# Optimization experiments

Measured on AMD Instinct MI355X. Metric: run time of the kernel, lower is better.

The kernel has to match this reference:

```python
import jax, jax.numpy as jnp
import numpy as np

N = 1_000_000
H = 128
G = 4096


def setup_inputs() -> dict:
    key = jax.random.key(0)
    k1, k2, k3, k4 = jax.random.split(key, 4)
    x = jax.random.normal(k1, (N, H), dtype=jnp.float32)
    batch = jnp.sort(jax.random.randint(k2, (N,), 0, G, dtype=jnp.int64))
    w1 = jax.random.normal(k3, (H, H), dtype=jnp.float32) * 0.05
    b1 = jnp.zeros((H,), dtype=jnp.float32)
    w2 = jax.random.normal(k4, (H, 1), dtype=jnp.float32) * 0.05
    b2 = jnp.zeros((1,), dtype=jnp.float32)
    return {"x": x, "batch": batch, "w1": w1, "b1": b1, "w2": w2, "b2": b2, "num_graphs": G}


def reference(x, batch, w1, b1, w2, b2, num_graphs):
    # attention MLP: Linear -> Tanh -> Linear(->1)
    s = (jnp.tanh(x @ w1 + b1) @ w2 + b2)[:, 0]  # [N]
    # segmented (per-graph) stable softmax
    smax = jax.ops.segment_max(s, batch, num_segments=num_graphs)  # [G]
    smax = jnp.where(jnp.isfinite(smax), smax, 0.0)  # guard empty graphs
    e = jnp.exp(s - smax[batch])  # [N]
    denom = jax.ops.segment_sum(e, batch, num_segments=num_graphs)  # [G]
    w = e / jnp.where(denom > 0, denom, 1.0)[batch]  # [N]
    # weighted sum pooling per graph -> [G, H]
    pooled = jax.ops.segment_sum(x * w[:, None], batch, num_segments=num_graphs)
    return pooled
```

## Files before the change

kernel.cpp:

```cpp
#include <hip/hip_runtime.h>
#include <math.h>

#define H 128

typedef float f32x4 __attribute__((ext_vector_type(4)));
typedef __bf16 bf16x8 __attribute__((ext_vector_type(8)));

__device__ __forceinline__ float fast_tanh(float v) {
    float e = __expf(2.0f * v);
    float r = __builtin_amdgcn_rcpf(e + 1.0f);
    return fmaf(-2.0f, r, 1.0f);
}

__global__ __launch_bounds__(256, 2) void k_compute_s_mfma(
    const float* __restrict__ x, const float* __restrict__ w1,
    const float* __restrict__ b1, const float* __restrict__ w2,
    const float* __restrict__ b2, float* __restrict__ s, int n, int ntiles)
{
    __shared__ __bf16 wsm[2 * H * H];

    const int tid = threadIdx.x;

    for (int idx = tid; idx < H * H; idx += 256) {
        int k = idx >> 7, nn = idx & 127;
        float v = w1[idx];
        __bf16 h = (__bf16)v;
        __bf16 l = (__bf16)(v - (float)h);
        int c = (k >> 3) ^ (nn & 15);
        int pos = nn * H + c * 8 + (k & 7);
        wsm[pos] = h;
        wsm[H * H + pos] = l;
    }

    const int wv = tid >> 6;
    const int lane = tid & 63;
    const int p = lane & 15;
    const int q = lane >> 4;

    float b1v[8], w2v[8];
    #pragma unroll
    for (int nt = 0; nt < 8; ++nt) {
        b1v[nt] = b1[nt * 16 + p];
        w2v[nt] = w2[nt * 16 + p];
    }
    const float b2v = b2[0];

    __syncthreads();

    for (int tile = blockIdx.x; tile < ntiles; tile += (int)gridDim.x) {
        const long long base = (long long)tile * 128 + wv * 32;

        bf16x8 ah[2][4], al[2][4];
        #pragma unroll
        for (int mt = 0; mt < 2; ++mt) {
            long long r = base + mt * 16 + p;
            const float4* rp = (const float4*)(x + r * H);
            const bool ok = (r < (long long)n);
            #pragma unroll
            for (int kc = 0; kc < 4; ++kc) {
                float4 u0 = {0.f, 0.f, 0.f, 0.f}, u1 = {0.f, 0.f, 0.f, 0.f};
                if (ok) { u0 = rp[kc * 8 + q * 2]; u1 = rp[kc * 8 + q * 2 + 1]; }
                float vals[8] = {u0.x, u0.y, u0.z, u0.w, u1.x, u1.y, u1.z, u1.w};
                #pragma unroll
                for (int j = 0; j < 8; ++j) {
                    __bf16 h = (__bf16)vals[j];
                    ah[mt][kc][j] = h;
                    al[mt][kc][j] = (__bf16)(vals[j] - (float)h);
                }
            }
        }

        f32x4 acc[2][8];
        #pragma unroll
        for (int mt = 0; mt < 2; ++mt)
            #pragma unroll
            for (int nt = 0; nt < 8; ++nt)
                acc[mt][nt] = (f32x4){0.f, 0.f, 0.f, 0.f};

        #pragma unroll
        for (int nt = 0; nt < 8; ++nt) {
            const int nn = nt * 16 + p;
            #pragma unroll
            for (int kc = 0; kc < 4; ++kc) {
                const int c = (kc * 4 + q) ^ p;
                const __bf16* bb = &wsm[nn * H + c * 8];
                bf16x8 bh = *(const bf16x8*)bb;
                bf16x8 bl = *(const bf16x8*)(bb + H * H);
                acc[0][nt] = __builtin_amdgcn_mfma_f32_16x16x32_bf16(ah[0][kc], bh, acc[0][nt], 0, 0, 0);
                acc[1][nt] = __builtin_amdgcn_mfma_f32_16x16x32_bf16(ah[1][kc], bh, acc[1][nt], 0, 0, 0);
                acc[0][nt] = __builtin_amdgcn_mfma_f32_16x16x32_bf16(al[0][kc], bh, acc[0][nt], 0, 0, 0);
                acc[1][nt] = __builtin_amdgcn_mfma_f32_16x16x32_bf16(al[1][kc], bh, acc[1][nt], 0, 0, 0);
                acc[0][nt] = __builtin_amdgcn_mfma_f32_16x16x32_bf16(ah[0][kc], bl, acc[0][nt], 0, 0, 0);
                acc[1][nt] = __builtin_amdgcn_mfma_f32_16x16x32_bf16(ah[1][kc], bl, acc[1][nt], 0, 0, 0);
            }
        }

        #pragma unroll
        for (int mt = 0; mt < 2; ++mt) {
            float part[4] = {0.f, 0.f, 0.f, 0.f};
            #pragma unroll
            for (int nt = 0; nt < 8; ++nt) {
                #pragma unroll
                for (int rg = 0; rg < 4; ++rg) {
                    float hv = fast_tanh(acc[mt][nt][rg] + b1v[nt]);
                    part[rg] = fmaf(hv, w2v[nt], part[rg]);
                }
            }
            #pragma unroll
            for (int off = 1; off < 16; off <<= 1) {
                #pragma unroll
                for (int rg = 0; rg < 4; ++rg)
                    part[rg] += __shfl_xor(part[rg], off);
            }
            if (p == 0) {
                #pragma unroll
                for (int rg = 0; rg < 4; ++rg) {
                    long long row = base + mt * 16 + q * 4 + rg;
                    if (row < (long long)n) s[row] = part[rg] + b2v;
                }
            }
        }
    }
}

__global__ void k_offsets(const int* __restrict__ batch, int n, int g_count,
                          int* __restrict__ offs)
{
    int g = blockIdx.x * blockDim.x + threadIdx.x;
    if (g > g_count) return;
    const bool is64 = (batch[n - 1] == 0);
    int lo = 0, hi = n;
    while (lo < hi) {
        int mid = (lo + hi) >> 1;
        int v = is64 ? batch[2 * mid] : batch[mid];
        if (v < g) lo = mid + 1; else hi = mid;
    }
    offs[g] = lo;
}

__global__ void k_stats(const float* __restrict__ s, const int* __restrict__ offs,
                        float* __restrict__ smax, float* __restrict__ sinv)
{
    const int g = blockIdx.x;
    const int lane = threadIdx.x;
    const int start = offs[g], end = offs[g + 1];
    float m = -INFINITY;
    for (int i = start + lane; i < end; i += 64) m = fmaxf(m, s[i]);
    #pragma unroll
    for (int off = 32; off; off >>= 1) m = fmaxf(m, __shfl_xor(m, off));
    if (!(m >= -3.0e38f)) m = 0.0f;
    float d = 0.0f;
    for (int i = start + lane; i < end; i += 64) d += __expf(s[i] - m);
    #pragma unroll
    for (int off = 32; off; off >>= 1) d += __shfl_xor(d, off);
    if (lane == 0) {
        smax[g] = m;
        sinv[g] = (d > 0.0f) ? (1.0f / d) : 1.0f;
    }
}

__global__ __launch_bounds__(256) void k_pool(
    const float* __restrict__ x, const float* __restrict__ s,
    const int* __restrict__ offs, const float* __restrict__ smax,
    const float* __restrict__ sinv, float* __restrict__ out)
{
    const int g = blockIdx.x;
    const int tid = threadIdx.x;
    const int rr = tid >> 5;
    const int c4 = tid & 31;
    const int start = offs[g], end = offs[g + 1];
    const float m = smax[g];
    const float inv = sinv[g];
    float4 acc = {0.f, 0.f, 0.f, 0.f};
    for (int i = start + rr; i < end; i += 8) {
        float w = __expf(s[i] - m) * inv;
        float4 xv = ((const float4*)(x + (size_t)i * H))[c4];
        acc.x = fmaf(w, xv.x, acc.x);
        acc.y = fmaf(w, xv.y, acc.y);
        acc.z = fmaf(w, xv.z, acc.z);
        acc.w = fmaf(w, xv.w, acc.w);
    }
    __shared__ float4 red[8][32];
    red[rr][c4] = acc;
    __syncthreads();
    if (rr == 0) {
        float4 t = red[0][c4];
        #pragma unroll
        for (int j = 1; j < 8; ++j) {
            float4 u = red[j][c4];
            t.x += u.x; t.y += u.y; t.z += u.z; t.w += u.w;
        }
        ((float4*)(out + (size_t)g * H))[c4] = t;
    }
}

extern "C" void kernel_launch(void* const* d_in, const int* in_sizes, int n_in,
                              void* d_out, int out_size, void* d_ws, size_t ws_size,
                              hipStream_t stream)
{
    const float* x     = (const float*)d_in[0];
    const int*   batch = (const int*)d_in[1];
    const float* w1    = (const float*)d_in[2];
    const float* b1    = (const float*)d_in[3];
    const float* w2    = (const float*)d_in[4];
    const float* b2    = (const float*)d_in[5];
    const int n = in_sizes[0] / H;
    const int G = out_size / H;
    float* out = (float*)d_out;

    float* s    = (float*)d_ws;
    float* smax = s + n;
    float* sinv = smax + G;
    int*   offs = (int*)(sinv + G);

    const int tiles = (n + 127) / 128;
    k_compute_s_mfma<<<1024, 256, 0, stream>>>(x, w1, b1, w2, b2, s, n, tiles);
    k_offsets<<<(G + 1 + 255) / 256, 256, 0, stream>>>(batch, n, G, offs);
    k_stats<<<G, 64, 0, stream>>>(s, offs, smax, sinv);
    k_pool<<<G, 256, 0, stream>>>(x, s, offs, smax, sinv, out);
}
```

Before: 1.030 ms.

## Shrink MFMA accumulator live range, enlarge blocks, fuse stats into pooling kernel

The score kernel now reduces each 16-column output tile through tanh and w2 right after its MFMA chain, so only two accumulators stay live instead of sixteen. This frees registers, and the block size rises to 512 threads with a launch bound of four blocks per CU. The separate softmax-stats kernel is merged into the pooling kernel using a block-wide max/sum reduction, which removes a launch and the smax/sinv round trip through memory. The trade-off is less MFMA interleaving per tile and b1/w2 loads inside the tile loop.

```diff
diff --git a/kernel.cpp b/kernel.cpp
--- a/kernel.cpp
+++ b/kernel.cpp
@@ -12,7 +12,7 @@
     return fmaf(-2.0f, r, 1.0f);
 }
 
-__global__ __launch_bounds__(256, 2) void k_compute_s_mfma(
+__global__ __launch_bounds__(512, 4) void k_compute_s_mfma(
     const float* __restrict__ x, const float* __restrict__ w1,
     const float* __restrict__ b1, const float* __restrict__ w2,
     const float* __restrict__ b2, float* __restrict__ s, int n, int ntiles)
@@ -21,7 +21,7 @@
 
     const int tid = threadIdx.x;
 
-    for (int idx = tid; idx < H * H; idx += 256) {
+    for (int idx = tid; idx < H * H; idx += 512) {
         int k = idx >> 7, nn = idx & 127;
         float v = w1[idx];
         __bf16 h = (__bf16)v;
@@ -36,19 +36,12 @@
     const int lane = tid & 63;
     const int p = lane & 15;
     const int q = lane >> 4;
-
-    float b1v[8], w2v[8];
-    #pragma unroll
-    for (int nt = 0; nt < 8; ++nt) {
-        b1v[nt] = b1[nt * 16 + p];
-        w2v[nt] = w2[nt * 16 + p];
-    }
     const float b2v = b2[0];
 
     __syncthreads();
 
     for (int tile = blockIdx.x; tile < ntiles; tile += (int)gridDim.x) {
-        const long long base = (long long)tile * 128 + wv * 32;
+        const long long base = (long long)tile * 256 + wv * 32;
 
         bf16x8 ah[2][4], al[2][4];
         #pragma unroll
@@ -70,55 +63,51 @@
             }
         }
 
-        f32x4 acc[2][8];
-        #pragma unroll
-        for (int mt = 0; mt < 2; ++mt)
-            #pragma unroll
-            for (int nt = 0; nt < 8; ++nt)
-                acc[mt][nt] = (f32x4){0.f, 0.f, 0.f, 0.f};
+        float part[2][4] = {{0.f, 0.f, 0.f, 0.f}, {0.f, 0.f, 0.f, 0.f}};
 
         #pragma unroll
         for (int nt = 0; nt < 8; ++nt) {
             const int nn = nt * 16 + p;
+            f32x4 acc0 = {0.f, 0.f, 0.f, 0.f};
+            f32x4 acc1 = {0.f, 0.f, 0.f, 0.f};
             #pragma unroll
             for (int kc = 0; kc < 4; ++kc) {
                 const int c = (kc * 4 + q) ^ p;
                 const __bf16* bb = &wsm[nn * H + c * 8];
                 bf16x8 bh = *(const bf16x8*)bb;
                 bf16x8 bl = *(const bf16x8*)(bb + H * H);
-                acc[0][nt] = __builtin_amdgcn_mfma_f32_16x16x32_bf16(ah[0][kc], bh, acc[0][nt], 0, 0, 0);
-                acc[1][nt] = __builtin_amdgcn_mfma_f32_16x16x32_bf16(ah[1][kc], bh, acc[1][nt], 0, 0, 0);
-                acc[0][nt] = __builtin_amdgcn_mfma_f32_16x16x32_bf16(al[0][kc], bh, acc[0][nt], 0, 0, 0);
-                acc[1][nt] = __builtin_amdgcn_mfma_f32_16x16x32_bf16(al[1][kc], bh, acc[1][nt], 0, 0, 0);
-                acc[0][nt] = __builtin_amdgcn_mfma_f32_16x16x32_bf16(ah[0][kc], bl, acc[0][nt], 0, 0, 0);
-                acc[1][nt] = __builtin_amdgcn_mfma_f32_16x16x32_bf16(ah[1][kc], bl, acc[1][nt], 0, 0, 0);
+                acc0 = __builtin_amdgcn_mfma_f32_16x16x32_bf16(ah[0][kc], bh, acc0, 0, 0, 0);
+                acc1 = __builtin_amdgcn_mfma_f32_16x16x32_bf16(ah[1][kc], bh, acc1, 0, 0, 0);
+                acc0 = __builtin_amdgcn_mfma_f32_16x16x32_bf16(al[0][kc], bh, acc0, 0, 0, 0);
+                acc1 = __builtin_amdgcn_mfma_f32_16x16x32_bf16(al[1][kc], bh, acc1, 0, 0, 0);
+                acc0 = __builtin_amdgcn_mfma_f32_16x16x32_bf16(ah[0][kc], bl, acc0, 0, 0, 0);
+                acc1 = __builtin_amdgcn_mfma_f32_16x16x32_bf16(ah[1][kc], bl, acc1, 0, 0, 0);
             }
-        }
-
-        #pragma unroll
-        for (int mt = 0; mt < 2; ++mt) {
-            float part[4] = {0.f, 0.f, 0.f, 0.f};
-            #pragma unroll
-            for (int nt = 0; nt < 8; ++nt) {
-                #pragma unroll
-                for (int rg = 0; rg < 4; ++rg) {
-                    float hv = fast_tanh(acc[mt][nt][rg] + b1v[nt]);
-                    part[rg] = fmaf(hv, w2v[nt], part[rg]);
-                }
+            const float b1v = b1[nn];
+            const float w2v = w2[nn];
+            #pragma unroll
+            for (int rg = 0; rg < 4; ++rg) {
+                part[0][rg] = fmaf(fast_tanh(acc0[rg] + b1v), w2v, part[0][rg]);
+                part[1][rg] = fmaf(fast_tanh(acc1[rg] + b1v), w2v, part[1][rg]);
             }
-            #pragma unroll
-            for (int off = 1; off < 16; off <<= 1) {
+        }
+
+        #pragma unroll
+        for (int off = 1; off < 16; off <<= 1) {
+            #pragma unroll
+            for (int mt = 0; mt < 2; ++mt)
                 #pragma unroll
                 for (int rg = 0; rg < 4; ++rg)
-                    part[rg] += __shfl_xor(part[rg], off);
-            }
-            if (p == 0) {
+                    part[mt][rg] += __shfl_xor(part[mt][rg], off);
+        }
+        if (p == 0) {
+            #pragma unroll
+            for (int mt = 0; mt < 2; ++mt)
                 #pragma unroll
                 for (int rg = 0; rg < 4; ++rg) {
                     long long row = base + mt * 16 + q * 4 + rg;
-                    if (row < (long long)n) s[row] = part[rg] + b2v;
+                    if (row < (long long)n) s[row] = part[mt][rg] + b2v;
                 }
-            }
         }
     }
 }
@@ -138,40 +127,39 @@
     offs[g] = lo;
 }
 
-__global__ void k_stats(const float* __restrict__ s, const int* __restrict__ offs,
-                        float* __restrict__ smax, float* __restrict__ sinv)
+__global__ __launch_bounds__(256) void k_stats_pool(
+    const float* __restrict__ x, const float* __restrict__ s,
+    const int* __restrict__ offs, float* __restrict__ out)
 {
     const int g = blockIdx.x;
-    const int lane = threadIdx.x;
+    const int tid = threadIdx.x;
     const int start = offs[g], end = offs[g + 1];
+
+    __shared__ float redm[4], redd[4];
+    __shared__ float4 red[8][32];
+
     float m = -INFINITY;
-    for (int i = start + lane; i < end; i += 64) m = fmaxf(m, s[i]);
+    for (int i = start + tid; i < end; i += 256) m = fmaxf(m, s[i]);
     #pragma unroll
     for (int off = 32; off; off >>= 1) m = fmaxf(m, __shfl_xor(m, off));
+    if ((tid & 63) == 0) redm[tid >> 6] = m;
+    __syncthreads();
+    m = fmaxf(fmaxf(redm[0], redm[1]), fmaxf(redm[2], redm[3]));
     if (!(m >= -3.0e38f)) m = 0.0f;
+
     float d = 0.0f;
-    for (int i = start + lane; i < end; i += 64) d += __expf(s[i] - m);
+    for (int i = start + tid; i < end; i += 256) d += __expf(s[i] - m);
     #pragma unroll
     for (int off = 32; off; off >>= 1) d += __shfl_xor(d, off);
-    if (lane == 0) {
-        smax[g] = m;
-        sinv[g] = (d > 0.0f) ? (1.0f / d) : 1.0f;
-    }
-}
-
-__global__ __launch_bounds__(256) void k_pool(
-    const float* __restrict__ x, const float* __restrict__ s,
-    const int* __restrict__ offs, const float* __restrict__ smax,
-    const float* __restrict__ sinv, float* __restrict__ out)
-{
-    const int g = blockIdx.x;
-    const int tid = threadIdx.x;
+    if ((tid & 63) == 0) redd[tid >> 6] = d;
+    __syncthreads();
+    d = redd[0] + redd[1] + redd[2] + redd[3];
+    const float inv = (d > 0.0f) ? (1.0f / d) : 1.0f;
+
     const int rr = tid >> 5;
     const int c4 = tid & 31;
-    const int start = offs[g], end = offs[g + 1];
-    const float m = smax[g];
-    const float inv = sinv[g];
     float4 acc = {0.f, 0.f, 0.f, 0.f};
+    #pragma unroll 2
     for (int i = start + rr; i < end; i += 8) {
         float w = __expf(s[i] - m) * inv;
         float4 xv = ((const float4*)(x + (size_t)i * H))[c4];
@@ -180,7 +168,6 @@
         acc.z = fmaf(w, xv.z, acc.z);
         acc.w = fmaf(w, xv.w, acc.w);
     }
-    __shared__ float4 red[8][32];
     red[rr][c4] = acc;
     __syncthreads();
     if (rr == 0) {
@@ -209,13 +196,10 @@
     float* out = (float*)d_out;
 
     float* s    = (float*)d_ws;
-    float* smax = s + n;
-    float* sinv = smax + G;
-    int*   offs = (int*)(sinv + G);
-
-    const int tiles = (n + 127) / 128;
-    k_compute_s_mfma<<<1024, 256, 0, stream>>>(x, w1, b1, w2, b2, s, n, tiles);
+    int*   offs = (int*)(s + n);
+
+    const int tiles = (n + 255) / 256;
+    k_compute_s_mfma<<<1024, 512, 0, stream>>>(x, w1, b1, w2, b2, s, n, tiles);
     k_offsets<<<(G + 1 + 255) / 256, 256, 0, stream>>>(batch, n, G, offs);
-    k_stats<<<G, 64, 0, stream>>>(s, offs, smax, sinv);
-    k_pool<<<G, 256, 0, stream>>>(x, s, offs, smax, sinv, out);
-}
+    k_stats_pool<<<G, 256, 0, stream>>>(x, s, offs, out);
+}
```

Measured after the change: 1.207 ms. 17.2% more time.
